# Optimization experiments

Measured on AMD Instinct MI355X. Metric: run time of the kernel, lower is better.

The kernel has to match this reference:

```python
import jax, jax.numpy as jnp
import numpy as np

B, T, D, H = 4, 2048, 1024, 16
DK = D // H


def setup_inputs() -> dict:
    key = jax.random.key(0)
    ks = jax.random.split(key, 9)
    s = 1.0 / np.sqrt(D)
    x = jax.random.normal(ks[0], (B, T, D), dtype=jnp.float32)
    mask = jnp.tril(jnp.ones((T, T), dtype=bool))[None, None]  # causal [1,1,T,T]
    wq = jax.random.uniform(ks[1], (D, D), jnp.float32, -s, s)
    bq = jax.random.uniform(ks[2], (D,), jnp.float32, -s, s)
    wk = jax.random.uniform(ks[3], (D, D), jnp.float32, -s, s)
    bk = jax.random.uniform(ks[4], (D,), jnp.float32, -s, s)
    wv = jax.random.uniform(ks[5], (D, D), jnp.float32, -s, s)
    bv = jax.random.uniform(ks[6], (D,), jnp.float32, -s, s)
    wo = jax.random.uniform(ks[7], (D, D), jnp.float32, -s, s)
    bo = jax.random.uniform(ks[8], (D,), jnp.float32, -s, s)
    return {"x": x, "mask": mask, "wq": wq, "bq": bq, "wk": wk, "bk": bk,
            "wv": wv, "bv": bv, "wo": wo, "bo": bo}


def reference(x, mask, wq, bq, wk, bk, wv, bv, wo, bo):
    # projections: torch Linear is x @ W.T + b; here weights stored as (D, D) used directly
    q = (x @ wq + bq).reshape(B, T, H, DK).transpose(0, 2, 1, 3)  # [B,H,T,dk]
    k = (x @ wk + bk).reshape(B, T, H, DK).transpose(0, 2, 1, 3)
    v = (x @ wv + bv).reshape(B, T, H, DK).transpose(0, 2, 1, 3)
    scores = jnp.einsum('bhqd,bhkd->bhqk', q, k) / jnp.sqrt(jnp.float32(DK))
    scores = jnp.where(mask, scores, -jnp.inf)
    attn = jax.nn.softmax(scores, axis=-1)
    # dropout p=0.0 -> identity
    y = jnp.einsum('bhqk,bhkd->bhqd', attn, v)
    y = y.transpose(0, 2, 1, 3).reshape(B, T, D)
    return y @ wo + bo
```

## Files before the change

### kernel.cpp

```cpp
#include <hip/hip_runtime.h>


typedef short s16x8 __attribute__((ext_vector_type(8)));
typedef short s16x4 __attribute__((ext_vector_type(4)));
typedef float f32x4 __attribute__((ext_vector_type(4)));
typedef unsigned int u32x2 __attribute__((ext_vector_type(2)));
typedef unsigned short u16x4 __attribute__((ext_vector_type(4)));

static __device__ __forceinline__ float bf2f(unsigned short u) {
    return __uint_as_float(((unsigned int)u) << 16);
}
static __device__ __forceinline__ unsigned short f2bf(float f) {
    unsigned int x = __float_as_uint(f);
    unsigned int r = x + 0x7fffu + ((x >> 16) & 1u);
    return (unsigned short)(r >> 16);
}

static __device__ __forceinline__ void gload_lds16(const short* g, short* l) {
    __builtin_amdgcn_global_load_lds((__attribute__((address_space(1))) void*)g,
                                     (__attribute__((address_space(3))) void*)l, 16, 0, 0);
}

static __device__ __forceinline__ unsigned int cvt_pk_bf16(float a, float b) {
    unsigned int r;
    asm("v_cvt_pk_bf16_f32 %0, %1, %2" : "=v"(r) : "v"(a), "v"(b));
    return r;
}

static __device__ __forceinline__ float fexp2(float x) {
    float r;
    asm("v_exp_f32 %0, %1" : "=v"(r) : "v"(x));
    return r;
}

__global__ __launch_bounds__(256) void prep(const void* __restrict__ x,
                                            const void* __restrict__ b0, const void* __restrict__ b1,
                                            const void* __restrict__ b2, const void* __restrict__ b3,
                                            const void* __restrict__ w0, const void* __restrict__ w1,
                                            const void* __restrict__ w2, const void* __restrict__ w3,
                                            unsigned short* __restrict__ xb,
                                            unsigned short* __restrict__ bb,
                                            unsigned short* __restrict__ wT,
                                            int* __restrict__ flag) {
    __shared__ unsigned short t[32][33];
    __shared__ int sflag;
    int bid = blockIdx.x, tid = threadIdx.x;

    {
        const unsigned short* xs = (const unsigned short*)x;
        bool big = false;
        for (int k = 0; k < 16; ++k) {
            float v = bf2f(xs[tid * 16 + k]);
            big |= !(fabsf(v) < 1e10f);
        }
        unsigned long long m = __ballot(big);
        if (tid == 0) sflag = 0;
        __syncthreads();
        if ((tid & 63) == 0 && m != 0ull) sflag = 1;
        __syncthreads();
    }
    int f = sflag;
    if (bid == 0 && tid == 0) *flag = f;

    if (bid < 8192) {
        int i = bid * 256 + tid;
        u16x4 o;
        if (f) {
            float4 v = ((const float4*)x)[i];
            o[0] = f2bf(v.x); o[1] = f2bf(v.y); o[2] = f2bf(v.z); o[3] = f2bf(v.w);
        } else {
            o = ((const u16x4*)x)[i];
        }
        ((u16x4*)xb)[i] = o;
    } else if (bid < 8208) {
        int i = (bid - 8192) * 256 + tid;
        const void* src = (i < 1024) ? b0 : (i < 2048 ? b1 : (i < 3072 ? b2 : b3));
        int k = i & 1023;
        bb[i] = f ? f2bf(((const float*)src)[k]) : ((const unsigned short*)src)[k];
    } else {
        int tz = bid - 8208;
        int z = tz >> 10, tile = tz & 1023;
        const void* src = (z == 0) ? w0 : (z == 1 ? w1 : (z == 2 ? w2 : w3));
        unsigned short* dst = wT + (size_t)z * 1024 * 1024;
        int xx = tid & 31, yy = tid >> 5;
        int n0 = (tile & 31) * 32, k0 = (tile >> 5) * 32;
        for (int j = 0; j < 32; j += 8) {
            size_t idx = (size_t)(k0 + yy + j) * 1024 + n0 + xx;
            t[yy + j][xx] = f ? f2bf(((const float*)src)[idx]) : ((const unsigned short*)src)[idx];
        }
        __syncthreads();
        for (int j = 0; j < 32; j += 8) dst[(size_t)(n0 + yy + j) * 1024 + k0 + xx] = t[xx][yy + j];
    }
}

__global__ __launch_bounds__(256) void gemm_bf16(const short* __restrict__ A,
                                                 const short* __restrict__ Bt,
                                                 void* __restrict__ C,
                                                 short* __restrict__ vt,
                                                 const unsigned short* __restrict__ bq,
                                                 const unsigned short* __restrict__ bk,
                                                 const unsigned short* __restrict__ bv,
                                                 int K, int ldc,
                                                 const int* __restrict__ flag, int f32out,
                                                 int scale_q, int fuse_v) {
    __shared__ __align__(16) short As[2][128][64];
    __shared__ __align__(16) short Bs[2][128][64];
    int tid = threadIdx.x;
    int wid = tid >> 6, lane = tid & 63, quad = lane >> 4, l16 = lane & 15;
    int wm = wid & 1, wn = wid >> 1;
    int m0 = blockIdx.x * 128, n0 = blockIdx.y * 128;
    bool wf = f32out && (*flag != 0);

    int srow = lane >> 3;
    int schunk = (lane & 7) ^ srow;
    const short* Ag = A  + (size_t)(m0 + wid * 32 + srow) * K + schunk * 8;
    const short* Bg = Bt + (size_t)(n0 + wid * 32 + srow) * K + schunk * 8;

    f32x4 acc[4][4] = {};
    int nt = K >> 6;

#pragma unroll
    for (int c = 0; c < 4; ++c) {
        gload_lds16(Ag + c * 8 * K, &As[0][wid * 32 + c * 8][0]);
        gload_lds16(Bg + c * 8 * K, &Bs[0][wid * 32 + c * 8][0]);
    }
    __syncthreads();

    for (int t = 0; t < nt; ++t) {
        if (t + 1 < nt) {
            int bu = (t + 1) & 1;
            int kof = (t + 1) * 64;
#pragma unroll
            for (int c = 0; c < 4; ++c) {
                gload_lds16(Ag + kof + c * 8 * K, &As[bu][wid * 32 + c * 8][0]);
                gload_lds16(Bg + kof + c * 8 * K, &Bs[bu][wid * 32 + c * 8][0]);
            }
        }
        const short (*Ab)[64] = As[t & 1];
#pragma unroll
        for (int kk = 0; kk < 2; ++kk) {
            s16x8 a[4], b[4];
#pragma unroll
            for (int i = 0; i < 4; ++i) {
                int row = wm * 64 + i * 16 + l16;
                a[i] = *(const s16x8*)&Ab[row][(((kk << 2) + quad) ^ (row & 7)) << 3];
            }
#pragma unroll
            for (int j = 0; j < 4; ++j) {
                int row = wn * 64 + j * 16 + l16;
                b[j] = *(const s16x8*)&Bs[t & 1][row][(((kk << 2) + quad) ^ (row & 7)) << 3];
            }
            __builtin_amdgcn_s_setprio(1);
#pragma unroll
            for (int i = 0; i < 4; ++i)
#pragma unroll
                for (int j = 0; j < 4; ++j)
                    acc[i][j] = __builtin_amdgcn_mfma_f32_16x16x32_bf16(a[i], b[j], acc[i][j], 0, 0, 0);
            __builtin_amdgcn_s_setprio(0);
        }
        __syncthreads();
    }
    for (int j = 0; j < 4; ++j) {
        int col = n0 + wn * 64 + j * 16 + l16;
        const unsigned short* bptr = (col < 1024) ? bq : (col < 2048 ? bk : bv);
        float bias = bf2f(bptr[col & 1023]);
        float cs = (scale_q && col < 1024) ? 0.18033688f : 1.0f;
        for (int i = 0; i < 4; ++i) {
            int rbase = m0 + wm * 64 + i * 16 + quad * 4;
            if (fuse_v && col >= 2048) {
                int h = (col - 2048) >> 6, dk = col & 63;
                int bb_ = rbase >> 11, t = rbase & 2047;
                s16x4 pk;
                for (int r = 0; r < 4; ++r) pk[r] = (short)f2bf(acc[i][j][r] + bias);
                *(s16x4*)(vt + ((size_t)((bb_ * 16 + h) * 64 + dk)) * 2048 + t) = pk;
            } else {
                for (int r = 0; r < 4; ++r) {
                    float v = (acc[i][j][r] + bias) * cs;
                    size_t idx = (size_t)(rbase + r) * ldc + col;
                    if (wf) ((float*)C)[idx] = v;
                    else    ((unsigned short*)C)[idx] = f2bf(v);
                }
            }
        }
    }
}

static __device__ __forceinline__ void stage_tiles(const short* kbase, const short* vbase,
                                                   int kt, short* Kb, short* Vb,
                                                   int wid, int lane) {
    int row = wid * 8 + (lane >> 3);
    int c_src = (lane & 7) ^ (lane >> 3);
    const short* kg = kbase + (size_t)(kt * 64 + row) * 3072 + c_src * 8;
    const short* vg = vbase + (size_t)row * 2048 + kt * 64 + c_src * 8;
    gload_lds16(kg, Kb + wid * 512);
    gload_lds16(vg, Vb + wid * 512);
}

static __device__ __forceinline__ s16x8 lds_frag(const short* buf, int row, int cg) {
    int slot = cg ^ (row & 7);
    return *(const s16x8*)(buf + row * 64 + slot * 8);
}

__global__ __launch_bounds__(512, 4) void attn(const short* __restrict__ qkv,
                                               const short* __restrict__ vt,
                                               unsigned short* __restrict__ y) {
    __shared__ __align__(16) short Kbuf[3][64 * 64];
    __shared__ __align__(16) short Vbuf[3][64 * 64];
    __shared__ __align__(16) short Ps[8][16 * 68];
    int tid = threadIdx.x;
    int wid = tid >> 6, lane = tid & 63, quad = lane >> 4, l16 = lane & 15;
    int bh = blockIdx.x, b = bh >> 4, h = bh & 15;
    const short* kbase = qkv + (size_t)b * 2048 * 3072 + 1024 + h * 64;
    const short* vbase = vt + (size_t)bh * 64 * 2048;
    short* PsW = &Ps[wid][0];

    s16x8 ones;
    for (int e = 0; e < 8; ++e) ones[e] = (short)0x3F80;

    int qb = 15 - (int)blockIdx.y;
    int ktmax = 2 * qb + 1;
    int kmax_w = 2 * qb + (wid >> 2);

    const short* qp = qkv + (size_t)(b * 2048 + qb * 128 + wid * 16 + l16) * 3072 + h * 64;
    s16x8 q0 = *(const s16x8*)(qp + quad * 8);
    s16x8 q1 = *(const s16x8*)(qp + 32 + quad * 8);

    float m_old = -INFINITY;
    f32x4 lacc = {0.f, 0.f, 0.f, 0.f};
    f32x4 o[4] = {};

    stage_tiles(kbase, vbase, 0, &Kbuf[0][0], &Vbuf[0][0], wid, lane);
    stage_tiles(kbase, vbase, 1, &Kbuf[1][0], &Vbuf[1][0], wid, lane);
    int ss = 2;
    int cc = 0;

    for (int kt = 0; kt <= ktmax; ++kt) {
        if (kt < ktmax) asm volatile("s_waitcnt vmcnt(2)" ::: "memory");
        else            asm volatile("s_waitcnt vmcnt(0)" ::: "memory");
        __builtin_amdgcn_sched_barrier(0);
        __builtin_amdgcn_s_barrier();

        if (kt + 2 <= ktmax) {
            stage_tiles(kbase, vbase, kt + 2, &Kbuf[0][0] + ss * 4096, &Vbuf[0][0] + ss * 4096,
                        wid, lane);
            ss = (ss == 2) ? 0 : ss + 1;
        }

        if (kt <= kmax_w) {
            const short* Kb = &Kbuf[0][0] + cc * 4096;
            const short* Vb = &Vbuf[0][0] + cc * 4096;

            f32x4 s[4] = {};
            __builtin_amdgcn_s_setprio(1);
            for (int j = 0; j < 4; ++j) {
                s16x8 klo = lds_frag(Kb, j * 16 + l16, quad);
                s16x8 khi = lds_frag(Kb, j * 16 + l16, 4 + quad);
                s[j] = __builtin_amdgcn_mfma_f32_16x16x32_bf16(klo, q0, s[j], 0, 0, 0);
                s[j] = __builtin_amdgcn_mfma_f32_16x16x32_bf16(khi, q1, s[j], 0, 0, 0);
            }
            __builtin_amdgcn_s_setprio(0);

            if (kt == kmax_w) {
                int qq = (wid & 3) * 16 + l16;
                for (int j = 0; j < 4; ++j)
                    for (int r = 0; r < 4; ++r)
                        if (j * 16 + quad * 4 + r > qq) s[j][r] = -INFINITY;
            }

            float mj0 = fmaxf(fmaxf(s[0][0], s[0][1]), s[0][2]);
            mj0 = fmaxf(mj0, s[0][3]);
            float mj1 = fmaxf(fmaxf(s[1][0], s[1][1]), s[1][2]);
            mj1 = fmaxf(mj1, s[1][3]);
            float mj2 = fmaxf(fmaxf(s[2][0], s[2][1]), s[2][2]);
            mj2 = fmaxf(mj2, s[2][3]);
            float mj3 = fmaxf(fmaxf(s[3][0], s[3][1]), s[3][2]);
            mj3 = fmaxf(mj3, s[3][3]);
            float mx = fmaxf(fmaxf(fmaxf(mj0, mj1), mj2), mj3);
            mx = fmaxf(mx, __shfl_xor(mx, 16));
            mx = fmaxf(mx, __shfl_xor(mx, 32));

            if (__any(mx > m_old + 8.0f)) {
                float mn = fmaxf(m_old, mx);
                float alpha = fexp2(m_old - mn);
                m_old = mn;
                float ar[4];
                for (int r = 0; r < 4; ++r) ar[r] = __shfl(alpha, quad * 4 + r);
                for (int r = 0; r < 4; ++r) {
                    lacc[r] *= ar[r];
                    for (int d = 0; d < 4; ++d) o[d][r] *= ar[r];
                }
            }

            for (int j = 0; j < 4; ++j) {
                float p0 = fexp2(s[j][0] - m_old);
                float p1 = fexp2(s[j][1] - m_old);
                float p2 = fexp2(s[j][2] - m_old);
                float p3 = fexp2(s[j][3] - m_old);
                u32x2 w;
                w.x = cvt_pk_bf16(p0, p1);
                w.y = cvt_pk_bf16(p2, p3);
                *(u32x2*)(PsW + l16 * 68 + j * 16 + quad * 4) = w;
            }

            s16x8 pa0 = *(const s16x8*)&PsW[l16 * 68 + quad * 8];
            s16x8 pa1 = *(const s16x8*)&PsW[l16 * 68 + 32 + quad * 8];
            __builtin_amdgcn_s_setprio(1);
            lacc = __builtin_amdgcn_mfma_f32_16x16x32_bf16(pa0, ones, lacc, 0, 0, 0);
            lacc = __builtin_amdgcn_mfma_f32_16x16x32_bf16(pa1, ones, lacc, 0, 0, 0);
            for (int d = 0; d < 4; ++d) {
                s16x8 vlo = lds_frag(Vb, d * 16 + l16, quad);
                s16x8 vhi = lds_frag(Vb, d * 16 + l16, 4 + quad);
                o[d] = __builtin_amdgcn_mfma_f32_16x16x32_bf16(pa0, vlo, o[d], 0, 0, 0);
                o[d] = __builtin_amdgcn_mfma_f32_16x16x32_bf16(pa1, vhi, o[d], 0, 0, 0);
            }
            __builtin_amdgcn_s_setprio(0);
        }
        cc = (cc == 2) ? 0 : cc + 1;
    }

    for (int r = 0; r < 4; ++r) {
        float inv = 1.f / lacc[r];
        int t = qb * 128 + wid * 16 + quad * 4 + r;
        for (int d = 0; d < 4; ++d)
            y[(size_t)(b * 2048 + t) * 1024 + h * 64 + d * 16 + l16] = f2bf(o[d][r] * inv);
    }
}

extern "C" void kernel_launch(void* const* d_in, const int* in_sizes, int n_in,
                              void* d_out, int out_size, void* d_ws, size_t ws_size,
                              hipStream_t stream) {
    (void)in_sizes; (void)n_in; (void)out_size; (void)ws_size;
    const void* x  = d_in[0];
    const void* wq = d_in[2]; const void* bq = d_in[3];
    const void* wk = d_in[4]; const void* bk = d_in[5];
    const void* wv = d_in[6]; const void* bv = d_in[7];
    const void* wo = d_in[8]; const void* bo = d_in[9];

    const size_t MB = 1024 * 1024;
    char* ws = (char*)d_ws;
    unsigned short* wT  = (unsigned short*)ws;
    short* qkv = (short*)(ws + 8 * MB);
    short* vt  = (short*)(ws + 56 * MB);
    unsigned short* xb = (unsigned short*)(ws + 72 * MB);
    unsigned short* yb = (unsigned short*)(ws + 72 * MB);
    unsigned short* bb = (unsigned short*)(ws + 88 * MB);
    int* flag = (int*)(ws + 88 * MB + 64 * 1024);

    prep<<<12304, 256, 0, stream>>>(x, bq, bk, bv, bo, wq, wk, wv, wo, xb, bb, wT, flag);

    gemm_bf16<<<dim3(64, 24), 256, 0, stream>>>((const short*)xb, (const short*)wT,
                                                qkv, vt, bb, bb + 1024, bb + 2048,
                                                1024, 3072, flag, 0, 1, 1);
    attn<<<dim3(64, 16), 512, 0, stream>>>(qkv, vt, yb);
    gemm_bf16<<<dim3(64, 8), 256, 0, stream>>>((const short*)yb, (const short*)(wT + 3072 * 1024),
                                               d_out, nullptr, bb + 3072, bb + 3072, bb + 3072,
                                               1024, 1024, flag, 1, 0, 0);
}
```

Before: 291.0 us.

## Swizzle GEMM block order and stage V-transpose epilogue through LDS

Remaps the flat workgroup index with an interleave of 8 so that concurrently running blocks share A/B tiles in cache. For the fused V output, it writes bias-added tiles into LDS in transposed layout and then emits contiguous 16-byte stores to the transposed V buffer, replacing the scattered 8-byte strided stores. The swizzle hardcodes 64 M-blocks and assumes the grid size is divisible by 8, and the epilogue reuses the As/Bs buffers, which adds an extra barrier.

```diff
diff --git a/kernel.cpp b/kernel.cpp
--- a/kernel.cpp
+++ b/kernel.cpp
@@ -108,7 +108,11 @@
     int tid = threadIdx.x;
     int wid = tid >> 6, lane = tid & 63, quad = lane >> 4, l16 = lane & 15;
     int wm = wid & 1, wn = wid >> 1;
-    int m0 = blockIdx.x * 128, n0 = blockIdx.y * 128;
+
+    int flat = blockIdx.y * 64 + blockIdx.x;
+    int nwg = gridDim.x * gridDim.y;
+    int swz = (flat & 7) * (nwg >> 3) + (flat >> 3);
+    int m0 = (swz & 63) * 128, n0 = (swz >> 6) * 128;
     bool wf = f32out && (*flag != 0);
 
     int srow = lane >> 3;
@@ -160,20 +164,39 @@
         }
         __syncthreads();
     }
-    for (int j = 0; j < 4; ++j) {
-        int col = n0 + wn * 64 + j * 16 + l16;
-        const unsigned short* bptr = (col < 1024) ? bq : (col < 2048 ? bk : bv);
-        float bias = bf2f(bptr[col & 1023]);
-        float cs = (scale_q && col < 1024) ? 0.18033688f : 1.0f;
-        for (int i = 0; i < 4; ++i) {
-            int rbase = m0 + wm * 64 + i * 16 + quad * 4;
-            if (fuse_v && col >= 2048) {
-                int h = (col - 2048) >> 6, dk = col & 63;
-                int bb_ = rbase >> 11, t = rbase & 2047;
+
+    if (fuse_v && n0 >= 2048) {
+        short* vtl = (wn == 0) ? (short*)As : (short*)Bs;
+#pragma unroll
+        for (int j = 0; j < 4; ++j) {
+            int c = j * 16 + l16;
+            float bias = bf2f(bv[(n0 - 2048) + wn * 64 + c]);
+#pragma unroll
+            for (int i = 0; i < 4; ++i) {
+                int row = wm * 64 + i * 16 + quad * 4;
                 s16x4 pk;
                 for (int r = 0; r < 4; ++r) pk[r] = (short)f2bf(acc[i][j][r] + bias);
-                *(s16x4*)(vt + ((size_t)((bb_ * 16 + h) * 64 + dk)) * 2048 + t) = pk;
-            } else {
+                *(s16x4*)(vtl + c * 136 + row) = pk;
+            }
+        }
+        __syncthreads();
+        int sel = tid >> 7, t2 = tid & 127;
+        int c = t2 >> 1, tc = (t2 & 1) * 64;
+        const short* vs = (sel ? (const short*)Bs : (const short*)As) + c * 136 + tc;
+        int hgl = ((n0 - 2048) >> 6) + sel;
+        int b_ = m0 >> 11;
+        short* gdst = vt + ((size_t)((b_ * 16 + hgl) * 64 + c)) * 2048 + (m0 & 2047) + tc;
+#pragma unroll
+        for (int e = 0; e < 8; ++e)
+            ((s16x8*)gdst)[e] = ((const s16x8*)vs)[e];
+    } else {
+        for (int j = 0; j < 4; ++j) {
+            int col = n0 + wn * 64 + j * 16 + l16;
+            const unsigned short* bptr = (col < 1024) ? bq : (col < 2048 ? bk : bv);
+            float bias = bf2f(bptr[col & 1023]);
+            float cs = (scale_q && col < 1024) ? 0.18033688f : 1.0f;
+            for (int i = 0; i < 4; ++i) {
+                int rbase = m0 + wm * 64 + i * 16 + quad * 4;
                 for (int r = 0; r < 4; ++r) {
                     float v = (acc[i][j][r] + bias) * cs;
                     size_t idx = (size_t)(rbase + r) * ldc + col;
```

Result: slower. 305.3 us (+4.9%).
